# Performance work log

Hardware: AMD Instinct MI355X
Metric: run time of the kernel (lower is better)

## Reference

```python
import jax, jax.numpy as jnp
import numpy as np

NUM_HEADS = 8


def _conv1x1(x, W, b):
    # 1x1 conv == per-pixel linear: x [N,C,H,W], W [O,C], b [O]
    return jnp.einsum('nchw,oc->nohw', x, W) + b[None, :, None, None]


def setup_inputs() -> dict:
    key = jax.random.key(0)
    ks = jax.random.split(key, 10)
    C = 512
    s = 1.0 / np.sqrt(C)  # keep pre-softmax logits in a sane range
    return {
        'x': jax.random.normal(ks[0], (2, C, 64, 64), dtype=jnp.float32),
        'Wq': jax.random.normal(ks[1], (C, C), dtype=jnp.float32) * s,
        'bq': jax.random.normal(ks[2], (C,), dtype=jnp.float32) * 0.01,
        'Wk': jax.random.normal(ks[3], (C, C), dtype=jnp.float32) * s,
        'bk': jax.random.normal(ks[4], (C,), dtype=jnp.float32) * 0.01,
        'Wv': jax.random.normal(ks[5], (C, C), dtype=jnp.float32) * s,
        'bv': jax.random.normal(ks[6], (C,), dtype=jnp.float32) * 0.01,
        'Wo': jax.random.normal(ks[7], (C, C), dtype=jnp.float32) * s,
        'bo': jax.random.normal(ks[8], (C,), dtype=jnp.float32) * 0.01,
        'gamma': jax.random.normal(ks[9], (1,), dtype=jnp.float32),
    }


def reference(x, Wq, bq, Wk, bk, Wv, bv, Wo, bo, gamma):
    N, C, H, W = x.shape
    nh = NUM_HEADS
    hd = C // nh
    S = H * W
    scale = 1.0 / (hd ** 0.5)
    # Projections via 1x1 conv, then split heads over flattened spatial tokens
    Q = _conv1x1(x, Wq, bq).reshape(N, nh, hd, S).transpose(0, 1, 3, 2)  # [N,h,S,d]
    K = _conv1x1(x, Wk, bk).reshape(N, nh, hd, S)                         # [N,h,d,S]
    V = _conv1x1(x, Wv, bv).reshape(N, nh, hd, S).transpose(0, 1, 3, 2)  # [N,h,S,d]
    attn = jax.nn.softmax(jnp.einsum('nhsd,nhdt->nhst', Q, K) * scale, axis=-1)
    out = jnp.einsum('nhst,nhtd->nhsd', attn, V)                          # [N,h,S,d]
    out = out.transpose(0, 1, 3, 2).reshape(N, C, H, W)
    out = _conv1x1(out, Wo, bo)
    return gamma[0] * out + x
```

## Files before the change

kernel.cpp:

```cpp
#include <hip/hip_runtime.h>
#include <hip/hip_bf16.h>

typedef __attribute__((ext_vector_type(4))) float f32x4;
typedef __attribute__((ext_vector_type(16))) float f32x16;
typedef __attribute__((ext_vector_type(8))) short s16x8;
typedef __attribute__((ext_vector_type(4))) unsigned short us16x4;
typedef __attribute__((ext_vector_type(4))) unsigned int u32x4;

#define C_DIM 512
#define S_DIM 4096
#define NB 2
#define NH 8
#define HD 64

#define QSCALE 0.1803368801111244f

__device__ __forceinline__ unsigned short f2bf(float f) {
    union { float f; unsigned u; } v; v.f = f;
    unsigned r = v.u + 0x7FFFu + ((v.u >> 16) & 1u);
    return (unsigned short)(r >> 16);
}

__device__ __forceinline__ float dev_exp2(float x) {
    float r;
    asm("v_exp_f32 %0, %1" : "=v"(r) : "v"(x));
    return r;
}

__device__ __forceinline__ unsigned cvt_pk_bf16(float lo, float hi) {
    unsigned r;
    asm("v_cvt_pk_bf16_f32 %0, %1, %2" : "=v"(r) : "v"(lo), "v"(hi));
    return r;
}

__device__ __forceinline__ void lane_swap(unsigned& a, unsigned& b) {
    asm("v_permlane32_swap_b32 %0, %1" : "+v"(a), "+v"(b));
}

__global__ __launch_bounds__(256) void wconv_kernel(
    const float* __restrict__ Wq, const float* __restrict__ Wk,
    const float* __restrict__ Wv, const float* __restrict__ Wo,
    unsigned short* __restrict__ Wb) {
    int i = blockIdx.x * 256 + threadIdx.x;
    int y = blockIdx.y;
    const float* src = (y == 0) ? Wq : (y == 1) ? Wk : (y == 2) ? Wv : Wo;
    Wb[(size_t)y * 262144 + i] = f2bf(src[i]);
}

__global__ __launch_bounds__(256) void xpose_kernel(
    const float* __restrict__ x, unsigned short* __restrict__ Xt) {
    __shared__ float tile[32][33];
    int n = blockIdx.z;
    int s0 = blockIdx.x * 32;
    int c0 = blockIdx.y * 32;
    int tx = threadIdx.x & 31;
    int ty = threadIdx.x >> 5;
#pragma unroll
    for (int r = 0; r < 4; ++r) {
        int c = c0 + ty + r * 8;
        tile[ty + r * 8][tx] = x[((size_t)n * C_DIM + c) * S_DIM + s0 + tx];
    }
    __syncthreads();
#pragma unroll
    for (int r = 0; r < 4; ++r) {
        int s = s0 + ty + r * 8;
        Xt[((size_t)n * S_DIM + s) * C_DIM + c0 + tx] = f2bf(tile[tx][ty + r * 8]);
    }
}

__global__ __launch_bounds__(256) void qkv_gemm_kernel(
    const unsigned short* __restrict__ Wb, const unsigned short* __restrict__ Xt,
    const float* __restrict__ bq, const float* __restrict__ bk, const float* __restrict__ bv,
    unsigned short* __restrict__ Qt, unsigned short* __restrict__ Kt,
    unsigned short* __restrict__ Vb) {
    __shared__ unsigned short As[128 * 72];
    __shared__ unsigned short Bs[128 * 72];
    int w = blockIdx.z >> 1;
    int n = blockIdx.z & 1;
    const unsigned short* A = Wb + (size_t)w * 262144;
    const unsigned short* B = Xt + (size_t)n * S_DIM * C_DIM;
    int tid = threadIdx.x;
    int wid = tid >> 6, lane = tid & 63;
    int wm = wid >> 1, wn = wid & 1;
    int lr = lane & 15, lq = lane >> 4;
    int bm = blockIdx.y * 128, bt = blockIdx.x * 128;

    f32x4 zero = {0.f, 0.f, 0.f, 0.f};
    f32x4 acc[4][4];
#pragma unroll
    for (int i = 0; i < 4; ++i)
#pragma unroll
        for (int j = 0; j < 4; ++j) acc[i][j] = zero;

    for (int ks = 0; ks < 8; ++ks) {
#pragma unroll
        for (int q = 0; q < 4; ++q) {
            int cc = tid * 4 + q;
            int row = cc >> 3, col8 = (cc & 7) * 8;
            s16x8 av = *(const s16x8*)(A + (size_t)(bm + row) * C_DIM + ks * 64 + col8);
            *(s16x8*)&As[row * 72 + col8] = av;
            s16x8 bvv = *(const s16x8*)(B + (size_t)(bt + row) * C_DIM + ks * 64 + col8);
            *(s16x8*)&Bs[row * 72 + col8] = bvv;
        }
        __syncthreads();
#pragma unroll
        for (int kk = 0; kk < 2; ++kk) {
            s16x8 af[4], bf[4];
#pragma unroll
            for (int i = 0; i < 4; ++i)
                af[i] = *(const s16x8*)&As[(wm * 64 + i * 16 + lr) * 72 + kk * 32 + lq * 8];
#pragma unroll
            for (int j = 0; j < 4; ++j)
                bf[j] = *(const s16x8*)&Bs[(wn * 64 + j * 16 + lr) * 72 + kk * 32 + lq * 8];
#pragma unroll
            for (int i = 0; i < 4; ++i)
#pragma unroll
                for (int j = 0; j < 4; ++j)
                    acc[i][j] = __builtin_amdgcn_mfma_f32_16x16x32_bf16(af[i], bf[j], acc[i][j], 0, 0, 0);
        }
        __syncthreads();
    }

    const float* bias = (w == 0) ? bq : (w == 1) ? bk : bv;
#pragma unroll
    for (int i = 0; i < 4; ++i) {
        int obase = bm + wm * 64 + i * 16 + lq * 4;
#pragma unroll
        for (int j = 0; j < 4; ++j) {
            int t = bt + wn * 64 + j * 16 + lr;
            if (w == 0) {
                us16x4 pk;
#pragma unroll
                for (int r = 0; r < 4; ++r)
                    pk[r] = f2bf((acc[i][j][r] + bias[obase + r]) * QSCALE);
                int h = obase >> 6, d = obase & 63;
                *(us16x4*)&Qt[(((size_t)(n * NH + h) * S_DIM) + t) * HD + d] = pk;
            } else if (w == 1) {
                us16x4 pk;
#pragma unroll
                for (int r = 0; r < 4; ++r) pk[r] = f2bf(acc[i][j][r] + bias[obase + r]);
                int h = obase >> 6, d = obase & 63;
                *(us16x4*)&Kt[(((size_t)(n * NH + h) * S_DIM) + t) * HD + d] = pk;
            } else {
#pragma unroll
                for (int r = 0; r < 4; ++r) {
                    int o = obase + r;
                    Vb[((size_t)(n * C_DIM + o)) * S_DIM + t] = f2bf(acc[i][j][r] + bias[o]);
                }
            }
        }
    }
}

__global__ __launch_bounds__(256) void attn_kernel(
    const unsigned short* __restrict__ Qt, const unsigned short* __restrict__ Kt,
    const unsigned short* __restrict__ Vb, unsigned short* __restrict__ Ot) {
    __shared__ unsigned short Ks[64 * 64];
    __shared__ unsigned short Vs[64 * 64];
    int tid = threadIdx.x, wid = tid >> 6, lane = tid & 63;
    int l31 = lane & 31, hi = lane >> 5;

    int bidl = blockIdx.x;
    int swz = (bidl & 7) * 64 + (bidl >> 3);
    int nh = swz >> 5;
    int qb = swz & 31;
    int n = nh >> 3, h = nh & 7;
    int qrow0 = qb * 128 + wid * 32;

    const unsigned short* Qh = Qt + (size_t)nh * S_DIM * HD;
    const unsigned short* Kh = Kt + (size_t)nh * S_DIM * HD;
    const unsigned short* Vh = Vb + ((size_t)(n * C_DIM + h * HD)) * S_DIM;

    s16x8 qf[4];
#pragma unroll
    for (int s = 0; s < 4; ++s)
        qf[s] = *(const s16x8*)&Qh[((size_t)(qrow0 + l31)) * HD + s * 16 + hi * 8];

    s16x8 ones;
#pragma unroll
    for (int r = 0; r < 8; ++r) ones[r] = (short)0x3F80;

    f32x16 Oacc[2], Lacc;
#pragma unroll
    for (int jm = 0; jm < 2; ++jm)
#pragma unroll
        for (int r = 0; r < 16; ++r) Oacc[jm][r] = 0.f;
#pragma unroll
    for (int r = 0; r < 16; ++r) Lacc[r] = 0.f;

    int srow0 = tid >> 3, sslot = tid & 7;

    s16x8 kreg[2], vreg[2];
#pragma unroll
    for (int q = 0; q < 2; ++q) {
        int row = srow0 + q * 32;
        kreg[q] = *(const s16x8*)&Kh[((size_t)row) * HD + sslot * 8];
        vreg[q] = *(const s16x8*)&Vh[((size_t)row) * S_DIM + sslot * 8];
    }

    for (int kt = 0; kt < 64; ++kt) {
#pragma unroll
        for (int q = 0; q < 2; ++q) {
            int row = srow0 + q * 32;
            int ws = (sslot ^ (row & 7)) * 8;
            *(s16x8*)&Ks[row * 64 + ws] = kreg[q];
            *(s16x8*)&Vs[row * 64 + ws] = vreg[q];
        }
        __syncthreads();
        if (kt < 63) {
#pragma unroll
            for (int q = 0; q < 2; ++q) {
                int row = srow0 + q * 32;
                kreg[q] = *(const s16x8*)&Kh[((size_t)((kt + 1) * 64 + row)) * HD + sslot * 8];
                vreg[q] = *(const s16x8*)&Vh[((size_t)row) * S_DIM + (kt + 1) * 64 + sslot * 8];
            }
        }

        f32x16 s_[2];
#pragma unroll
        for (int jm = 0; jm < 2; ++jm) {
#pragma unroll
            for (int r = 0; r < 16; ++r) s_[jm][r] = 0.f;
            int arow = jm * 32 + l31;
            int sw = (arow & 7);
#pragma unroll
            for (int st = 0; st < 4; ++st) {
                s16x8 kf = *(const s16x8*)&Ks[arow * 64 + ((2 * st + hi) ^ sw) * 8];
                s_[jm] = __builtin_amdgcn_mfma_f32_32x32x16_bf16(kf, qf[st], s_[jm], 0, 0, 0);
            }
        }

        s16x8 pf[2][2];
#pragma unroll
        for (int jm = 0; jm < 2; ++jm) {
            unsigned pk0 = cvt_pk_bf16(dev_exp2(s_[jm][0]),  dev_exp2(s_[jm][1]));
            unsigned pk1 = cvt_pk_bf16(dev_exp2(s_[jm][2]),  dev_exp2(s_[jm][3]));
            unsigned pk2 = cvt_pk_bf16(dev_exp2(s_[jm][4]),  dev_exp2(s_[jm][5]));
            unsigned pk3 = cvt_pk_bf16(dev_exp2(s_[jm][6]),  dev_exp2(s_[jm][7]));
            unsigned pk4 = cvt_pk_bf16(dev_exp2(s_[jm][8]),  dev_exp2(s_[jm][9]));
            unsigned pk5 = cvt_pk_bf16(dev_exp2(s_[jm][10]), dev_exp2(s_[jm][11]));
            unsigned pk6 = cvt_pk_bf16(dev_exp2(s_[jm][12]), dev_exp2(s_[jm][13]));
            unsigned pk7 = cvt_pk_bf16(dev_exp2(s_[jm][14]), dev_exp2(s_[jm][15]));
            lane_swap(pk2, pk0);
            lane_swap(pk3, pk1);
            lane_swap(pk6, pk4);
            lane_swap(pk7, pk5);
            u32x4 w0 = {pk0, pk1, pk2, pk3};
            u32x4 w1 = {pk4, pk5, pk6, pk7};
            pf[jm][0] = __builtin_bit_cast(s16x8, w0);
            pf[jm][1] = __builtin_bit_cast(s16x8, w1);
        }

#pragma unroll
        for (int jm = 0; jm < 2; ++jm)
#pragma unroll
            for (int st = 0; st < 2; ++st)
                Lacc = __builtin_amdgcn_mfma_f32_32x32x16_bf16(ones, pf[jm][st], Lacc, 0, 0, 0);

#pragma unroll
        for (int jm2 = 0; jm2 < 2; ++jm2) {
            int vrow = jm2 * 32 + l31;
            int sw = (vrow & 7);
#pragma unroll
            for (int jm = 0; jm < 2; ++jm)
#pragma unroll
                for (int st = 0; st < 2; ++st) {
                    s16x8 vf = *(const s16x8*)&Vs[vrow * 64 + ((jm * 4 + st * 2 + hi) ^ sw) * 8];
                    Oacc[jm2] = __builtin_amdgcn_mfma_f32_32x32x16_bf16(vf, pf[jm][st], Oacc[jm2], 0, 0, 0);
                }
        }
        __syncthreads();
    }

    float inv = 1.f / Lacc[0];
    int token = qrow0 + l31;
    unsigned short* orow = Ot + ((size_t)n * S_DIM + token) * C_DIM + h * HD;
#pragma unroll
    for (int jm2 = 0; jm2 < 2; ++jm2)
#pragma unroll
        for (int rq = 0; rq < 4; ++rq) {
            int d = jm2 * 32 + 8 * rq + 4 * hi;
            us16x4 pk;
#pragma unroll
            for (int r = 0; r < 4; ++r) pk[r] = f2bf(Oacc[jm2][rq * 4 + r] * inv);
            *(us16x4*)&orow[d] = pk;
        }
}

__global__ __launch_bounds__(256) void out_gemm_kernel(
    const unsigned short* __restrict__ Wb, const unsigned short* __restrict__ Ot,
    const float* __restrict__ bo, const float* __restrict__ gamma,
    const float* __restrict__ xin, float* __restrict__ out) {
    __shared__ unsigned short As[128 * 72];
    __shared__ unsigned short Bs[128 * 72];
    int n = blockIdx.z;
    const unsigned short* A = Wb + (size_t)3 * 262144;
    const unsigned short* B = Ot + (size_t)n * S_DIM * C_DIM;
    int tid = threadIdx.x;
    int wid = tid >> 6, lane = tid & 63;
    int wm = wid >> 1, wn = wid & 1;
    int lr = lane & 15, lq = lane >> 4;
    int bm = blockIdx.y * 128, bt = blockIdx.x * 128;

    f32x4 zero = {0.f, 0.f, 0.f, 0.f};
    f32x4 acc[4][4];
#pragma unroll
    for (int i = 0; i < 4; ++i)
#pragma unroll
        for (int j = 0; j < 4; ++j) acc[i][j] = zero;

    for (int ks = 0; ks < 8; ++ks) {
#pragma unroll
        for (int q = 0; q < 4; ++q) {
            int cc = tid * 4 + q;
            int row = cc >> 3, col8 = (cc & 7) * 8;
            s16x8 av = *(const s16x8*)(A + (size_t)(bm + row) * C_DIM + ks * 64 + col8);
            *(s16x8*)&As[row * 72 + col8] = av;
            s16x8 bvv = *(const s16x8*)(B + (size_t)(bt + row) * C_DIM + ks * 64 + col8);
            *(s16x8*)&Bs[row * 72 + col8] = bvv;
        }
        __syncthreads();
#pragma unroll
        for (int kk = 0; kk < 2; ++kk) {
            s16x8 af[4], bf[4];
#pragma unroll
            for (int i = 0; i < 4; ++i)
                af[i] = *(const s16x8*)&As[(wm * 64 + i * 16 + lr) * 72 + kk * 32 + lq * 8];
#pragma unroll
            for (int j = 0; j < 4; ++j)
                bf[j] = *(const s16x8*)&Bs[(wn * 64 + j * 16 + lr) * 72 + kk * 32 + lq * 8];
#pragma unroll
            for (int i = 0; i < 4; ++i)
#pragma unroll
                for (int j = 0; j < 4; ++j)
                    acc[i][j] = __builtin_amdgcn_mfma_f32_16x16x32_bf16(af[i], bf[j], acc[i][j], 0, 0, 0);
        }
        __syncthreads();
    }

    float g = gamma[0];
#pragma unroll
    for (int i = 0; i < 4; ++i) {
        int obase = bm + wm * 64 + i * 16 + lq * 4;
#pragma unroll
        for (int j = 0; j < 4; ++j) {
            int t = bt + wn * 64 + j * 16 + lr;
#pragma unroll
            for (int r = 0; r < 4; ++r) {
                int o = obase + r;
                size_t idx = ((size_t)(n * C_DIM + o)) * S_DIM + t;
                out[idx] = g * (acc[i][j][r] + bo[o]) + xin[idx];
            }
        }
    }
}

extern "C" void kernel_launch(void* const* d_in, const int* in_sizes, int n_in,
                              void* d_out, int out_size, void* d_ws, size_t ws_size,
                              hipStream_t stream) {
    const float* x  = (const float*)d_in[0];
    const float* Wq = (const float*)d_in[1];
    const float* bq = (const float*)d_in[2];
    const float* Wk = (const float*)d_in[3];
    const float* bk = (const float*)d_in[4];
    const float* Wv = (const float*)d_in[5];
    const float* bv = (const float*)d_in[6];
    const float* Wo = (const float*)d_in[7];
    const float* bo = (const float*)d_in[8];
    const float* gamma = (const float*)d_in[9];
    float* out = (float*)d_out;

    char* ws = (char*)d_ws;
    unsigned short* Wb = (unsigned short*)ws;
    unsigned short* Xt = (unsigned short*)(ws + ((size_t)2  << 20));
    unsigned short* Qt = (unsigned short*)(ws + ((size_t)10 << 20));
    unsigned short* Kt = (unsigned short*)(ws + ((size_t)18 << 20));
    unsigned short* Vb = (unsigned short*)(ws + ((size_t)26 << 20));
    unsigned short* Ot = (unsigned short*)(ws + ((size_t)34 << 20));

    wconv_kernel<<<dim3(1024, 4), 256, 0, stream>>>(Wq, Wk, Wv, Wo, Wb);
    xpose_kernel<<<dim3(128, 16, 2), 256, 0, stream>>>(x, Xt);
    qkv_gemm_kernel<<<dim3(32, 4, 6), 256, 0, stream>>>(Wb, Xt, bq, bk, bv, Qt, Kt, Vb);
    attn_kernel<<<512, 256, 0, stream>>>(Qt, Kt, Vb, Ot);
    out_gemm_kernel<<<dim3(32, 4, 2), 256, 0, stream>>>(Wb, Ot, bo, gamma, x, out);
}
```

Before: 150.2 us.

## Split attention KV range across two blocks, add combine kernel, use direct global-to-LDS loads

Attention now splits each query block's key/value range into two halves processed by separate workgroups (1024 blocks instead of 512), writing unnormalized fp32 partial outputs and row sums that a new combine kernel adds and normalizes. This raises parallelism on the many-CU device at the cost of extra fp32 partial traffic and one more launch. It relies on the softmax not subtracting a running max, so the partials can simply be summed. The QKV and output GEMMs switch to global_load_lds direct copies into unpadded LDS tiles, and the K/V LDS swizzle gains an extra XOR term to reduce bank conflicts.

After: 156.1 us. 3.9% more time.

```diff
diff --git a/kernel.cpp b/kernel.cpp
--- a/kernel.cpp
+++ b/kernel.cpp
@@ -35,6 +35,12 @@
 
 __device__ __forceinline__ void lane_swap(unsigned& a, unsigned& b) {
     asm("v_permlane32_swap_b32 %0, %1" : "+v"(a), "+v"(b));
+}
+
+__device__ __forceinline__ void gload_lds16(const void* g, void* l) {
+    __builtin_amdgcn_global_load_lds(
+        (const __attribute__((address_space(1))) void*)g,
+        (__attribute__((address_space(3))) void*)l, 16, 0, 0);
 }
 
 __global__ __launch_bounds__(256) void wconv_kernel(
@@ -73,8 +79,8 @@
     const float* __restrict__ bq, const float* __restrict__ bk, const float* __restrict__ bv,
     unsigned short* __restrict__ Qt, unsigned short* __restrict__ Kt,
     unsigned short* __restrict__ Vb) {
-    __shared__ unsigned short As[128 * 72];
-    __shared__ unsigned short Bs[128 * 72];
+    __shared__ unsigned short As[128 * 64];
+    __shared__ unsigned short Bs[128 * 64];
     int w = blockIdx.z >> 1;
     int n = blockIdx.z & 1;
     const unsigned short* A = Wb + (size_t)w * 262144;
@@ -84,6 +90,7 @@
     int wm = wid >> 1, wn = wid & 1;
     int lr = lane & 15, lq = lane >> 4;
     int bm = blockIdx.y * 128, bt = blockIdx.x * 128;
+    int r_in = lane >> 3, c8 = (lane & 7) * 8;
 
     f32x4 zero = {0.f, 0.f, 0.f, 0.f};
     f32x4 acc[4][4];
@@ -95,12 +102,9 @@
     for (int ks = 0; ks < 8; ++ks) {
 #pragma unroll
         for (int q = 0; q < 4; ++q) {
-            int cc = tid * 4 + q;
-            int row = cc >> 3, col8 = (cc & 7) * 8;
-            s16x8 av = *(const s16x8*)(A + (size_t)(bm + row) * C_DIM + ks * 64 + col8);
-            *(s16x8*)&As[row * 72 + col8] = av;
-            s16x8 bvv = *(const s16x8*)(B + (size_t)(bt + row) * C_DIM + ks * 64 + col8);
-            *(s16x8*)&Bs[row * 72 + col8] = bvv;
+            int row = wid * 32 + q * 8;
+            gload_lds16(A + (size_t)(bm + row + r_in) * C_DIM + ks * 64 + c8, &As[row * 64]);
+            gload_lds16(B + (size_t)(bt + row + r_in) * C_DIM + ks * 64 + c8, &Bs[row * 64]);
         }
         __syncthreads();
 #pragma unroll
@@ -108,10 +112,10 @@
             s16x8 af[4], bf[4];
 #pragma unroll
             for (int i = 0; i < 4; ++i)
-                af[i] = *(const s16x8*)&As[(wm * 64 + i * 16 + lr) * 72 + kk * 32 + lq * 8];
+                af[i] = *(const s16x8*)&As[(wm * 64 + i * 16 + lr) * 64 + kk * 32 + lq * 8];
 #pragma unroll
             for (int j = 0; j < 4; ++j)
-                bf[j] = *(const s16x8*)&Bs[(wn * 64 + j * 16 + lr) * 72 + kk * 32 + lq * 8];
+                bf[j] = *(const s16x8*)&Bs[(wn * 64 + j * 16 + lr) * 64 + kk * 32 + lq * 8];
 #pragma unroll
             for (int i = 0; i < 4; ++i)
 #pragma unroll
@@ -154,18 +158,23 @@
 
 __global__ __launch_bounds__(256) void attn_kernel(
     const unsigned short* __restrict__ Qt, const unsigned short* __restrict__ Kt,
-    const unsigned short* __restrict__ Vb, unsigned short* __restrict__ Ot) {
+    const unsigned short* __restrict__ Vb, float* __restrict__ Opart,
+    float* __restrict__ Lpart) {
     __shared__ unsigned short Ks[64 * 64];
     __shared__ unsigned short Vs[64 * 64];
     int tid = threadIdx.x, wid = tid >> 6, lane = tid & 63;
     int l31 = lane & 31, hi = lane >> 5;
+    int radj = (l31 & 7) ^ ((l31 >> 3) & 3);
 
     int bidl = blockIdx.x;
-    int swz = (bidl & 7) * 64 + (bidl >> 3);
-    int nh = swz >> 5;
-    int qb = swz & 31;
+    int swz = (bidl & 7) * 128 + (bidl >> 3);
+    int nh = swz >> 6;
+    int rem = swz & 63;
+    int qb = rem >> 1;
+    int half = rem & 1;
     int n = nh >> 3, h = nh & 7;
     int qrow0 = qb * 128 + wid * 32;
+    int kvbase = half * 2048;
 
     const unsigned short* Qh = Qt + (size_t)nh * S_DIM * HD;
     const unsigned short* Kh = Kt + (size_t)nh * S_DIM * HD;
@@ -173,8 +182,8 @@
 
     s16x8 qf[4];
 #pragma unroll
-    for (int s = 0; s < 4; ++s)
-        qf[s] = *(const s16x8*)&Qh[((size_t)(qrow0 + l31)) * HD + s * 16 + hi * 8];
+    for (int st = 0; st < 4; ++st)
+        qf[st] = *(const s16x8*)&Qh[((size_t)(qrow0 + l31)) * HD + st * 16 + hi * 8];
 
     s16x8 ones;
 #pragma unroll
@@ -189,30 +198,30 @@
     for (int r = 0; r < 16; ++r) Lacc[r] = 0.f;
 
     int srow0 = tid >> 3, sslot = tid & 7;
+    int wslot = (sslot ^ (srow0 & 7) ^ ((srow0 >> 3) & 3)) * 8;
 
     s16x8 kreg[2], vreg[2];
 #pragma unroll
     for (int q = 0; q < 2; ++q) {
         int row = srow0 + q * 32;
-        kreg[q] = *(const s16x8*)&Kh[((size_t)row) * HD + sslot * 8];
-        vreg[q] = *(const s16x8*)&Vh[((size_t)row) * S_DIM + sslot * 8];
-    }
-
-    for (int kt = 0; kt < 64; ++kt) {
+        kreg[q] = *(const s16x8*)&Kh[((size_t)(kvbase + row)) * HD + sslot * 8];
+        vreg[q] = *(const s16x8*)&Vh[((size_t)row) * S_DIM + kvbase + sslot * 8];
+    }
+
+    for (int kt = 0; kt < 32; ++kt) {
 #pragma unroll
         for (int q = 0; q < 2; ++q) {
             int row = srow0 + q * 32;
-            int ws = (sslot ^ (row & 7)) * 8;
-            *(s16x8*)&Ks[row * 64 + ws] = kreg[q];
-            *(s16x8*)&Vs[row * 64 + ws] = vreg[q];
-        }
-        __syncthreads();
-        if (kt < 63) {
+            *(s16x8*)&Ks[row * 64 + wslot] = kreg[q];
+            *(s16x8*)&Vs[row * 64 + wslot] = vreg[q];
+        }
+        __syncthreads();
+        if (kt < 31) {
 #pragma unroll
             for (int q = 0; q < 2; ++q) {
                 int row = srow0 + q * 32;
-                kreg[q] = *(const s16x8*)&Kh[((size_t)((kt + 1) * 64 + row)) * HD + sslot * 8];
-                vreg[q] = *(const s16x8*)&Vh[((size_t)row) * S_DIM + (kt + 1) * 64 + sslot * 8];
+                kreg[q] = *(const s16x8*)&Kh[((size_t)(kvbase + (kt + 1) * 64 + row)) * HD + sslot * 8];
+                vreg[q] = *(const s16x8*)&Vh[((size_t)row) * S_DIM + kvbase + (kt + 1) * 64 + sslot * 8];
             }
         }
 
@@ -222,10 +231,9 @@
 #pragma unroll
             for (int r = 0; r < 16; ++r) s_[jm][r] = 0.f;
             int arow = jm * 32 + l31;
-            int sw = (arow & 7);
 #pragma unroll
             for (int st = 0; st < 4; ++st) {
-                s16x8 kf = *(const s16x8*)&Ks[arow * 64 + ((2 * st + hi) ^ sw) * 8];
+                s16x8 kf = *(const s16x8*)&Ks[arow * 64 + ((2 * st + hi) ^ radj) * 8];
                 s_[jm] = __builtin_amdgcn_mfma_f32_32x32x16_bf16(kf, qf[st], s_[jm], 0, 0, 0);
             }
         }
@@ -260,39 +268,58 @@
 #pragma unroll
         for (int jm2 = 0; jm2 < 2; ++jm2) {
             int vrow = jm2 * 32 + l31;
-            int sw = (vrow & 7);
 #pragma unroll
             for (int jm = 0; jm < 2; ++jm)
 #pragma unroll
                 for (int st = 0; st < 2; ++st) {
-                    s16x8 vf = *(const s16x8*)&Vs[vrow * 64 + ((jm * 4 + st * 2 + hi) ^ sw) * 8];
+                    s16x8 vf = *(const s16x8*)&Vs[vrow * 64 + ((jm * 4 + st * 2 + hi) ^ radj) * 8];
                     Oacc[jm2] = __builtin_amdgcn_mfma_f32_32x32x16_bf16(vf, pf[jm][st], Oacc[jm2], 0, 0, 0);
                 }
         }
         __syncthreads();
     }
 
-    float inv = 1.f / Lacc[0];
     int token = qrow0 + l31;
-    unsigned short* orow = Ot + ((size_t)n * S_DIM + token) * C_DIM + h * HD;
+    float* obase = Opart + (((size_t)(half * 16 + nh) * S_DIM + token) * HD);
 #pragma unroll
     for (int jm2 = 0; jm2 < 2; ++jm2)
 #pragma unroll
         for (int rq = 0; rq < 4; ++rq) {
             int d = jm2 * 32 + 8 * rq + 4 * hi;
-            us16x4 pk;
-#pragma unroll
-            for (int r = 0; r < 4; ++r) pk[r] = f2bf(Oacc[jm2][rq * 4 + r] * inv);
-            *(us16x4*)&orow[d] = pk;
-        }
+            f32x4 v = {Oacc[jm2][rq * 4 + 0], Oacc[jm2][rq * 4 + 1],
+                       Oacc[jm2][rq * 4 + 2], Oacc[jm2][rq * 4 + 3]};
+            *(f32x4*)&obase[d] = v;
+        }
+    if (hi == 0)
+        Lpart[(size_t)(half * 16 + nh) * S_DIM + token] = Lacc[0];
+}
+
+__global__ __launch_bounds__(256) void combine_kernel(
+    const float* __restrict__ Opart, const float* __restrict__ Lpart,
+    unsigned short* __restrict__ Ot) {
+    int g = blockIdx.x * 256 + threadIdx.x;
+    int d4 = (g & 15) * 4;
+    int s = (g >> 4) & 4095;
+    int nh = g >> 16;
+    size_t base0 = ((size_t)nh * S_DIM + s) * HD + d4;
+    size_t base1 = base0 + (size_t)16 * S_DIM * HD;
+    f32x4 o0 = *(const f32x4*)&Opart[base0];
+    f32x4 o1 = *(const f32x4*)&Opart[base1];
+    float l = Lpart[(size_t)nh * S_DIM + s] + Lpart[(size_t)(16 + nh) * S_DIM + s];
+    float inv = 1.f / l;
+    int n = nh >> 3, h = nh & 7;
+    us16x4 pk;
+#pragma unroll
+    for (int r = 0; r < 4; ++r) pk[r] = f2bf((o0[r] + o1[r]) * inv);
+    *(us16x4*)&Ot[((size_t)n * S_DIM + s) * C_DIM + h * HD + d4] = pk;
 }
 
 __global__ __launch_bounds__(256) void out_gemm_kernel(
     const unsigned short* __restrict__ Wb, const unsigned short* __restrict__ Ot,
     const float* __restrict__ bo, const float* __restrict__ gamma,
     const float* __restrict__ xin, float* __restrict__ out) {
-    __shared__ unsigned short As[128 * 72];
-    __shared__ unsigned short Bs[128 * 72];
+    __shared__ unsigned short As[128 * 64];
+    __shared__ unsigned short Bs[128 * 64];
     int n = blockIdx.z;
     const unsigned short* A = Wb + (size_t)3 * 262144;
     const unsigned short* B = Ot + (size_t)n * S_DIM * C_DIM;
@@ -301,6 +328,7 @@
     int wm = wid >> 1, wn = wid & 1;
     int lr = lane & 15, lq = lane >> 4;
     int bm = blockIdx.y * 128, bt = blockIdx.x * 128;
+    int r_in = lane >> 3, c8 = (lane & 7) * 8;
 
     f32x4 zero = {0.f, 0.f, 0.f, 0.f};
     f32x4 acc[4][4];
@@ -312,12 +340,9 @@
     for (int ks = 0; ks < 8; ++ks) {
 #pragma unroll
         for (int q = 0; q < 4; ++q) {
-            int cc = tid * 4 + q;
-            int row = cc >> 3, col8 = (cc & 7) * 8;
-            s16x8 av = *(const s16x8*)(A + (size_t)(bm + row) * C_DIM + ks * 64 + col8);
-            *(s16x8*)&As[row * 72 + col8] = av;
-            s16x8 bvv = *(const s16x8*)(B + (size_t)(bt + row) * C_DIM + ks * 64 + col8);
-            *(s16x8*)&Bs[row * 72 + col8] = bvv;
+            int row = wid * 32 + q * 8;
+            gload_lds16(A + (size_t)(bm + row + r_in) * C_DIM + ks * 64 + c8, &As[row * 64]);
+            gload_lds16(B + (size_t)(bt + row + r_in) * C_DIM + ks * 64 + c8, &Bs[row * 64]);
         }
         __syncthreads();
 #pragma unroll
@@ -325,10 +350,10 @@
             s16x8 af[4], bf[4];
 #pragma unroll
             for (int i = 0; i < 4; ++i)
-                af[i] = *(const s16x8*)&As[(wm * 64 + i * 16 + lr) * 72 + kk * 32 + lq * 8];
+                af[i] = *(const s16x8*)&As[(wm * 64 + i * 16 + lr) * 64 + kk * 32 + lq * 8];
 #pragma unroll
             for (int j = 0; j < 4; ++j)
-                bf[j] = *(const s16x8*)&Bs[(wn * 64 + j * 16 + lr) * 72 + kk * 32 + lq * 8];
+                bf[j] = *(const s16x8*)&Bs[(wn * 64 + j * 16 + lr) * 64 + kk * 32 + lq * 8];
 #pragma unroll
             for (int i = 0; i < 4; ++i)
 #pragma unroll
@@ -377,10 +402,13 @@
     unsigned short* Kt = (unsigned short*)(ws + ((size_t)18 << 20));
     unsigned short* Vb = (unsigned short*)(ws + ((size_t)26 << 20));
     unsigned short* Ot = (unsigned short*)(ws + ((size_t)34 << 20));
+    float* Opart = (float*)(ws + ((size_t)42 << 20));
+    float* Lpart = (float*)(ws + ((size_t)76 << 20));
 
     wconv_kernel<<<dim3(1024, 4), 256, 0, stream>>>(Wq, Wk, Wv, Wo, Wb);
     xpose_kernel<<<dim3(128, 16, 2), 256, 0, stream>>>(x, Xt);
     qkv_gemm_kernel<<<dim3(32, 4, 6), 256, 0, stream>>>(Wb, Xt, bq, bk, bv, Qt, Kt, Vb);
-    attn_kernel<<<512, 256, 0, stream>>>(Qt, Kt, Vb, Ot);
+    attn_kernel<<<1024, 256, 0, stream>>>(Qt, Kt, Vb, Opart, Lpart);
+    combine_kernel<<<4096, 256, 0, stream>>>(Opart, Lpart, Ot);
     out_gemm_kernel<<<dim3(32, 4, 2), 256, 0, stream>>>(Wb, Ot, bo, gamma, x, out);
 }
```
